# Kernel optimization log

Measured on AMD Instinct MI355X. Metric: run time of the kernel, lower is better.

## Reference

```python
import jax, jax.numpy as jnp
import numpy as np

N_NODES = 50000
N_EDGES = 800000
H = 128   # atom_hidden_feats
B = 64    # bond_in_feats
NEG_SLOPE = 0.01  # torch LeakyReLU default


def setup_inputs() -> dict:
    key = jax.random.key(0)
    k1, k2, k3, k4, k5 = jax.random.split(key, 5)
    feat = jax.random.normal(k1, (N_NODES, H), dtype=jnp.float32)
    gdf_feat = jax.random.normal(k2, (N_EDGES, B), dtype=jnp.float32)
    # Linear(2H+B -> H): weight [H, 2H+B], bias [H]
    W = jax.random.normal(k3, (H, 2 * H + B), dtype=jnp.float32) * 0.05
    b = jnp.zeros((H,), dtype=jnp.float32)
    src = jax.random.randint(k4, (N_EDGES,), 0, N_NODES, dtype=jnp.int64)
    dst = jax.random.randint(k5, (N_EDGES,), 0, N_NODES, dtype=jnp.int64)
    return {"feat": feat, "gdf_feat": gdf_feat, "W": W, "b": b, "src": src, "dst": dst}


def reference(feat, gdf_feat, W, b, src, dst):
    n_nodes = feat.shape[0]
    # Per-edge message: concat(src_feat, dst_feat, edge_feat) -> linear -> gate
    z = jnp.concatenate([feat[src], feat[dst], gdf_feat], axis=-1)  # [E, 2H+B]
    z = z @ W.T + b                                                 # [E, H]
    msg = jax.nn.sigmoid(z) * jnp.where(z > 0, z, NEG_SLOPE * z)    # sigmoid * leaky_relu
    # Scatter-sum messages to destination nodes
    return jax.ops.segment_sum(msg, dst, num_segments=n_nodes)      # [N, H]
```

## Files before the change

kernel.cpp:

```cpp
#include <hip/hip_runtime.h>
#include <hip/hip_bf16.h>

typedef __attribute__((ext_vector_type(8)))  short bf16x8;
typedef __attribute__((ext_vector_type(16))) float f32x16;
typedef __attribute__((ext_vector_type(4)))  float f32x4;
typedef __attribute__((ext_vector_type(2)))  __fp16 fp16x2;

#define NN 50000
#define EE 800000
#define HH 128
#define KK 320
#define NEG 0.01f
#define NTILES (EE / 64)
#define NBLK 1024
#define ACC_BYTES ((size_t)NN * HH * 2)

__device__ __forceinline__ unsigned pack2(float a, float b) {
    unsigned short lo = __builtin_bit_cast(unsigned short, __float2bfloat16(a));
    unsigned short hi = __builtin_bit_cast(unsigned short, __float2bfloat16(b));
    return (unsigned)lo | ((unsigned)hi << 16);
}

__global__ __launch_bounds__(256) void featcvt_kernel(const float* __restrict__ feat,
                                                      ushort* __restrict__ featb)
{
    const int t = blockIdx.x * 256 + threadIdx.x;
    const float* p = feat + (long long)t * 8;
    f32x4 v0 = *(const f32x4*)p;
    f32x4 v1 = *(const f32x4*)(p + 4);
    int4 h;
    h.x = (int)pack2(v0[0], v0[1]); h.y = (int)pack2(v0[2], v0[3]);
    h.z = (int)pack2(v1[0], v1[1]); h.w = (int)pack2(v1[2], v1[3]);
    *(int4*)(featb + (long long)t * 8) = h;
}

template<int USE_F16, int FEATB>
__global__ __launch_bounds__(256, 4) void fused_edge_kernel(
    const float*  __restrict__ feat, const ushort* __restrict__ featb,
    const float*  __restrict__ gdf,
    const float*  __restrict__ W,    const float* __restrict__ bias,
    const int*    __restrict__ src,  const int*   __restrict__ dst,
    float* __restrict__ out, __fp16* __restrict__ acc16)
{
    __shared__ int4 lds4[64 * 40];
    char* lds = (char*)lds4;

    const int tid  = threadIdx.x;
    const int lane = tid & 63;
    const int wid  = tid >> 6;
    const int col  = wid * 32 + (lane & 31);
    const int khalf = lane >> 5;
    const int r = tid >> 2, q = tid & 3;

    bf16x8 Wb[20];
    {
        const float* wrow = W + col * KK + khalf * 8;
        #pragma unroll
        for (int k = 0; k < 20; k++) {
            f32x4 x0 = *(const f32x4*)(wrow + k * 16);
            f32x4 x1 = *(const f32x4*)(wrow + k * 16 + 4);
            union { bf16x8 v; unsigned u[4]; } t;
            t.u[0] = pack2(x0[0], x0[1]); t.u[1] = pack2(x0[2], x0[3]);
            t.u[2] = pack2(x1[0], x1[1]); t.u[3] = pack2(x1[2], x1[3]);
            Wb[k] = t.v;
        }
    }
    const float bv = bias[col];

    int tile = blockIdx.x;
    int sCur = src[(long long)tile * 64 + r];
    int dCur = dst[(long long)tile * 64 + r];

    while (tile < NTILES) {
        const long long ebase = (long long)tile * 64;

        {
            const float* ge = gdf + (ebase + r) * 64;
            if (FEATB) {
                const ushort* fs = featb + (long long)sCur * HH;
                const ushort* fd = featb + (long long)dCur * HH;
                #pragma unroll
                for (int i = 0; i < 8; i++) {
                    const int c = q + i * 4;
                    const ushort* p = (c < 16) ? (fs + c * 8) : (fd + (c - 16) * 8);
                    int4 h = *(const int4*)p;
                    *(int4*)(lds + r * 640 + ((c * 16) ^ ((r & 7) << 4))) = h;
                }
                #pragma unroll
                for (int i = 8; i < 10; i++) {
                    const int c = q + i * 4;
                    const float* p = ge + (c - 32) * 8;
                    f32x4 v0 = *(const f32x4*)p;
                    f32x4 v1 = *(const f32x4*)(p + 4);
                    int4 h;
                    h.x = (int)pack2(v0[0], v0[1]); h.y = (int)pack2(v0[2], v0[3]);
                    h.z = (int)pack2(v1[0], v1[1]); h.w = (int)pack2(v1[2], v1[3]);
                    *(int4*)(lds + r * 640 + ((c * 16) ^ ((r & 7) << 4))) = h;
                }
            } else {
                const float* fs = feat + (long long)sCur * HH;
                const float* fd = feat + (long long)dCur * HH;
                #pragma unroll
                for (int i = 0; i < 10; i++) {
                    const int c = q + i * 4;
                    const float* p = (c < 16) ? (fs + c * 8)
                                   : (c < 32) ? (fd + (c - 16) * 8)
                                              : (ge + (c - 32) * 8);
                    f32x4 v0 = *(const f32x4*)p;
                    f32x4 v1 = *(const f32x4*)(p + 4);
                    int4 h;
                    h.x = (int)pack2(v0[0], v0[1]); h.y = (int)pack2(v0[2], v0[3]);
                    h.z = (int)pack2(v1[0], v1[1]); h.w = (int)pack2(v1[2], v1[3]);
                    *(int4*)(lds + r * 640 + ((c * 16) ^ ((r & 7) << 4))) = h;
                }
            }
        }
        __syncthreads();

        const int nt = tile + NBLK;
        if (nt < NTILES) {
            sCur = src[(long long)nt * 64 + r];
            dCur = dst[(long long)nt * 64 + r];
        }

        f32x16 acc0 = {}; f32x16 acc1 = {};
        const int arow = lane & 31;
        const int xr   = (arow & 7) << 4;
        #pragma unroll
        for (int k = 0; k < 20; k++) {
            const int kb = k * 32 + khalf * 16;
            bf16x8 a0 = *(const bf16x8*)(lds + arow * 640 + (kb ^ xr));
            bf16x8 a1 = *(const bf16x8*)(lds + (arow + 32) * 640 + (kb ^ xr));
            acc0 = __builtin_amdgcn_mfma_f32_32x32x16_bf16(a0, Wb[k], acc0, 0, 0, 0);
            acc1 = __builtin_amdgcn_mfma_f32_32x32x16_bf16(a1, Wb[k], acc1, 0, 0, 0);
        }

        const int* dtile = dst + ebase;
        #pragma unroll
        for (int rt = 0; rt < 2; rt++) {
            const f32x16 A = rt ? acc1 : acc0;
            #pragma unroll
            for (int g = 0; g < 4; g++) {
                #pragma unroll
                for (int j = 0; j < 4; j++) {
                    const int reg = g * 4 + j;
                    const int row = j + g * 8 + khalf * 4;
                    const float z  = A[reg] + bv;
                    const float lr = z > 0.f ? z : NEG * z;
                    const float sg = 1.f / (1.f + __expf(-z));
                    const float m  = lr * sg;
                    const int dn = dtile[rt * 32 + row];
                    if (USE_F16) {
                        const float o = __shfl_xor(m, 1);
                        if (!(lane & 1)) {
                            fp16x2 hv = __builtin_amdgcn_cvt_pkrtz(m, o);
                            __fp16* p = acc16 + (long long)dn * HH + col;
                            asm volatile("global_atomic_pk_add_f16 %0, %1, off"
                                         :: "v"(p), "v"(hv) : "memory");
                        }
                    } else {
                        unsafeAtomicAdd(out + (long long)dn * HH + col, m);
                    }
                }
            }
        }
        __syncthreads();
        tile = nt;
    }
}

__global__ __launch_bounds__(256) void conv_kernel(const int4* __restrict__ acc,
                                                   float4* __restrict__ out)
{
    const int i = blockIdx.x * 256 + threadIdx.x;
    union { int4 v; __fp16 h[8]; } u;
    u.v = acc[i];
    float4 a, b;
    a.x = (float)u.h[0]; a.y = (float)u.h[1]; a.z = (float)u.h[2]; a.w = (float)u.h[3];
    b.x = (float)u.h[4]; b.y = (float)u.h[5]; b.z = (float)u.h[6]; b.w = (float)u.h[7];
    out[2 * i]     = a;
    out[2 * i + 1] = b;
}

extern "C" void kernel_launch(void* const* d_in, const int* in_sizes, int n_in,
                              void* d_out, int out_size, void* d_ws, size_t ws_size,
                              hipStream_t stream) {
    const float* feat = (const float*)d_in[0];
    const float* gdf  = (const float*)d_in[1];
    const float* W    = (const float*)d_in[2];
    const float* bias = (const float*)d_in[3];
    const int*   src  = (const int*)d_in[4];
    const int*   dst  = (const int*)d_in[5];
    float* out = (float*)d_out;

    __fp16* acc16 = (__fp16*)d_ws;
    ushort* featb = (ushort*)((char*)d_ws + ACC_BYTES);

    if (ws_size >= 2 * ACC_BYTES) {
        (void)hipMemsetAsync(d_ws, 0, ACC_BYTES, stream);
        featcvt_kernel<<<(NN * HH / 8) / 256 + 1, 256, 0, stream>>>(feat, featb);
        fused_edge_kernel<1, 1><<<NBLK, 256, 0, stream>>>(feat, featb, gdf, W, bias,
                                                          src, dst, out, acc16);
        conv_kernel<<<(NN * HH / 8) / 256, 256, 0, stream>>>((const int4*)d_ws,
                                                             (float4*)out);
    } else if (ws_size >= ACC_BYTES) {
        (void)hipMemsetAsync(d_ws, 0, ACC_BYTES, stream);
        fused_edge_kernel<1, 0><<<NBLK, 256, 0, stream>>>(feat, featb, gdf, W, bias,
                                                          src, dst, out, acc16);
        conv_kernel<<<(NN * HH / 8) / 256, 256, 0, stream>>>((const int4*)d_ws,
                                                             (float4*)out);
    } else {
        (void)hipMemsetAsync(out, 0, (size_t)out_size * sizeof(float), stream);
        fused_edge_kernel<0, 0><<<NBLK, 256, 0, stream>>>(feat, featb, gdf, W, bias,
                                                          src, dst, out, acc16);
    }
}
```

Before: 395.2 us.

## Double-buffer edge tiles in LDS and prefetch next tile's gathers into registers

The persistent edge kernel becomes a software pipeline. The next tile's feature gathers and gdf loads go into registers while the current tile's MFMA and atomic scatter run, then get written into a second LDS buffer. Destination indices are staged in LDS instead of being reloaded from global memory in the epilogue. The block count is halved, the occupancy hint drops to 2 blocks per SM, and the fallback paths are simplified into a non-persistent kernel. Register and LDS pressure go up, and the smaller grid may hide latency less well.

After: 355.4 us. -10.1%, faster.

```diff
diff --git a/kernel.cpp b/kernel.cpp
--- a/kernel.cpp
+++ b/kernel.cpp
@@ -12,7 +12,7 @@
 #define KK 320
 #define NEG 0.01f
 #define NTILES (EE / 64)
-#define NBLK 1024
+#define NBLK 512
 #define ACC_BYTES ((size_t)NN * HH * 2)
 
 __device__ __forceinline__ unsigned pack2(float a, float b) {
@@ -34,16 +34,14 @@
     *(int4*)(featb + (long long)t * 8) = h;
 }
 
-template<int USE_F16, int FEATB>
-__global__ __launch_bounds__(256, 4) void fused_edge_kernel(
-    const float*  __restrict__ feat, const ushort* __restrict__ featb,
-    const float*  __restrict__ gdf,
-    const float*  __restrict__ W,    const float* __restrict__ bias,
-    const int*    __restrict__ src,  const int*   __restrict__ dst,
-    float* __restrict__ out, __fp16* __restrict__ acc16)
-{
-    __shared__ int4 lds4[64 * 40];
-    char* lds = (char*)lds4;
+__global__ __launch_bounds__(256, 2) void fused_pipe_kernel(
+    const ushort* __restrict__ featb, const float* __restrict__ gdf,
+    const float*  __restrict__ W,     const float* __restrict__ bias,
+    const int*    __restrict__ src,   const int*   __restrict__ dst,
+    __fp16* __restrict__ acc16)
+{
+    __shared__ int4 lds4[2][64 * 40];
+    __shared__ int  dsts[2][64];
 
     const int tid  = threadIdx.x;
     const int lane = tid & 63;
@@ -67,75 +65,87 @@
     }
     const float bv = bias[col];
 
+    int4  sf[8];
+    f32x4 sg[4];
+    int   dStage;
+
+    auto issueLoads = [&](int t, int s_i, int d_i) {
+        const ushort* fs = featb + (long long)s_i * HH;
+        const ushort* fd = featb + (long long)d_i * HH;
+        const float*  ge = gdf + ((long long)t * 64 + r) * 64;
+        #pragma unroll
+        for (int i = 0; i < 8; i++) {
+            const int c = q + i * 4;
+            sf[i] = *(const int4*)((c < 16) ? (fs + c * 8) : (fd + (c - 16) * 8));
+        }
+        #pragma unroll
+        for (int i = 0; i < 2; i++) {
+            const int cg = q + i * 4;
+            sg[2 * i]     = *(const f32x4*)(ge + cg * 8);
+            sg[2 * i + 1] = *(const f32x4*)(ge + cg * 8 + 4);
+        }
+    };
+    auto writeStage = [&](int buf) {
+        char* base = (char*)lds4[buf];
+        const int xr = (r & 7) << 4;
+        #pragma unroll
+        for (int i = 0; i < 8; i++) {
+            const int c = q + i * 4;
+            *(int4*)(base + r * 640 + ((c * 16) ^ xr)) = sf[i];
+        }
+        #pragma unroll
+        for (int i = 0; i < 2; i++) {
+            const int c = 32 + q + i * 4;
+            int4 h;
+            h.x = (int)pack2(sg[2*i][0], sg[2*i][1]);
+            h.y = (int)pack2(sg[2*i][2], sg[2*i][3]);
+            h.z = (int)pack2(sg[2*i+1][0], sg[2*i+1][1]);
+            h.w = (int)pack2(sg[2*i+1][2], sg[2*i+1][3]);
+            *(int4*)(base + r * 640 + ((c * 16) ^ xr)) = h;
+        }
+        if (q == 0) dsts[buf][r] = dStage;
+    };
+
     int tile = blockIdx.x;
-    int sCur = src[(long long)tile * 64 + r];
-    int dCur = dst[(long long)tile * 64 + r];
-
-    while (tile < NTILES) {
-        const long long ebase = (long long)tile * 64;
-
-        {
-            const float* ge = gdf + (ebase + r) * 64;
-            if (FEATB) {
-                const ushort* fs = featb + (long long)sCur * HH;
-                const ushort* fd = featb + (long long)dCur * HH;
-                #pragma unroll
-                for (int i = 0; i < 8; i++) {
-                    const int c = q + i * 4;
-                    const ushort* p = (c < 16) ? (fs + c * 8) : (fd + (c - 16) * 8);
-                    int4 h = *(const int4*)p;
-                    *(int4*)(lds + r * 640 + ((c * 16) ^ ((r & 7) << 4))) = h;
-                }
-                #pragma unroll
-                for (int i = 8; i < 10; i++) {
-                    const int c = q + i * 4;
-                    const float* p = ge + (c - 32) * 8;
-                    f32x4 v0 = *(const f32x4*)p;
-                    f32x4 v1 = *(const f32x4*)(p + 4);
-                    int4 h;
-                    h.x = (int)pack2(v0[0], v0[1]); h.y = (int)pack2(v0[2], v0[3]);
-                    h.z = (int)pack2(v1[0], v1[1]); h.w = (int)pack2(v1[2], v1[3]);
-                    *(int4*)(lds + r * 640 + ((c * 16) ^ ((r & 7) << 4))) = h;
-                }
-            } else {
-                const float* fs = feat + (long long)sCur * HH;
-                const float* fd = feat + (long long)dCur * HH;
-                #pragma unroll
-                for (int i = 0; i < 10; i++) {
-                    const int c = q + i * 4;
-                    const float* p = (c < 16) ? (fs + c * 8)
-                                   : (c < 32) ? (fd + (c - 16) * 8)
-                                              : (ge + (c - 32) * 8);
-                    f32x4 v0 = *(const f32x4*)p;
-                    f32x4 v1 = *(const f32x4*)(p + 4);
-                    int4 h;
-                    h.x = (int)pack2(v0[0], v0[1]); h.y = (int)pack2(v0[2], v0[3]);
-                    h.z = (int)pack2(v1[0], v1[1]); h.w = (int)pack2(v1[2], v1[3]);
-                    *(int4*)(lds + r * 640 + ((c * 16) ^ ((r & 7) << 4))) = h;
-                }
-            }
-        }
-        __syncthreads();
-
-        const int nt = tile + NBLK;
-        if (nt < NTILES) {
-            sCur = src[(long long)nt * 64 + r];
-            dCur = dst[(long long)nt * 64 + r];
-        }
-
+    int sN = src[(long long)tile * 64 + r];
+    int dN = dst[(long long)tile * 64 + r];
+    issueLoads(tile, sN, dN);
+    dStage = dN;
+    int nt = tile + NBLK;
+    {
+        const int tc = (nt < NTILES) ? nt : 0;
+        sN = src[(long long)tc * 64 + r];
+        dN = dst[(long long)tc * 64 + r];
+    }
+    writeStage(0);
+    __syncthreads();
+
+    int cur = 0;
+    const int arow = lane & 31;
+    const int xa   = (arow & 7) << 4;
+
+    while (true) {
+        const bool hasNext = (nt < NTILES);
+        if (hasNext) {
+            issueLoads(nt, sN, dN);
+            dStage = dN;
+            const int nnt = nt + NBLK;
+            const int tc = (nnt < NTILES) ? nnt : 0;
+            sN = src[(long long)tc * 64 + r];
+            dN = dst[(long long)tc * 64 + r];
+        }
+
+        char* abase = (char*)lds4[cur];
         f32x16 acc0 = {}; f32x16 acc1 = {};
-        const int arow = lane & 31;
-        const int xr   = (arow & 7) << 4;
         #pragma unroll
         for (int k = 0; k < 20; k++) {
             const int kb = k * 32 + khalf * 16;
-            bf16x8 a0 = *(const bf16x8*)(lds + arow * 640 + (kb ^ xr));
-            bf16x8 a1 = *(const bf16x8*)(lds + (arow + 32) * 640 + (kb ^ xr));
+            bf16x8 a0 = *(const bf16x8*)(abase + arow * 640 + (kb ^ xa));
+            bf16x8 a1 = *(const bf16x8*)(abase + (arow + 32) * 640 + (kb ^ xa));
             acc0 = __builtin_amdgcn_mfma_f32_32x32x16_bf16(a0, Wb[k], acc0, 0, 0, 0);
             acc1 = __builtin_amdgcn_mfma_f32_32x32x16_bf16(a1, Wb[k], acc1, 0, 0, 0);
         }
 
-        const int* dtile = dst + ebase;
         #pragma unroll
         for (int rt = 0; rt < 2; rt++) {
             const f32x16 A = rt ? acc1 : acc0;
@@ -147,25 +157,101 @@
                     const int row = j + g * 8 + khalf * 4;
                     const float z  = A[reg] + bv;
                     const float lr = z > 0.f ? z : NEG * z;
-                    const float sg = 1.f / (1.f + __expf(-z));
-                    const float m  = lr * sg;
-                    const int dn = dtile[rt * 32 + row];
-                    if (USE_F16) {
-                        const float o = __shfl_xor(m, 1);
-                        if (!(lane & 1)) {
-                            fp16x2 hv = __builtin_amdgcn_cvt_pkrtz(m, o);
-                            __fp16* p = acc16 + (long long)dn * HH + col;
-                            asm volatile("global_atomic_pk_add_f16 %0, %1, off"
-                                         :: "v"(p), "v"(hv) : "memory");
-                        }
-                    } else {
-                        unsafeAtomicAdd(out + (long long)dn * HH + col, m);
+                    const float sg2 = 1.f / (1.f + __expf(-z));
+                    const float m  = lr * sg2;
+                    const float o  = __shfl_xor(m, 1);
+                    const int dn = dsts[cur][rt * 32 + row];
+                    if (!(lane & 1)) {
+                        fp16x2 hv = __builtin_amdgcn_cvt_pkrtz(m, o);
+                        __fp16* p = acc16 + (long long)dn * HH + col;
+                        asm volatile("global_atomic_pk_add_f16 %0, %1, off"
+                                     :: "v"(p), "v"(hv) : "memory");
                     }
                 }
             }
         }
+
+        if (!hasNext) break;
+        writeStage(cur ^ 1);
+        tile = nt; nt += NBLK; cur ^= 1;
         __syncthreads();
-        tile = nt;
+    }
+}
+
+__global__ __launch_bounds__(256) void fused_fallback_kernel(
+    const float* __restrict__ feat, const float* __restrict__ gdf,
+    const float* __restrict__ W,    const float* __restrict__ bias,
+    const int*   __restrict__ src,  const int*   __restrict__ dst,
+    float* __restrict__ out)
+{
+    __shared__ int4 lds4[64 * 40];
+    __shared__ int  dsts[64];
+    char* lds = (char*)lds4;
+    const int tid = threadIdx.x, lane = tid & 63, wid = tid >> 6;
+    const int col = wid * 32 + (lane & 31), khalf = lane >> 5;
+    const int r = tid >> 2, q = tid & 3;
+    const long long ebase = (long long)blockIdx.x * 64;
+
+    bf16x8 Wb[20];
+    {
+        const float* wrow = W + col * KK + khalf * 8;
+        #pragma unroll
+        for (int k = 0; k < 20; k++) {
+            f32x4 x0 = *(const f32x4*)(wrow + k * 16);
+            f32x4 x1 = *(const f32x4*)(wrow + k * 16 + 4);
+            union { bf16x8 v; unsigned u[4]; } t;
+            t.u[0] = pack2(x0[0], x0[1]); t.u[1] = pack2(x0[2], x0[3]);
+            t.u[2] = pack2(x1[0], x1[1]); t.u[3] = pack2(x1[2], x1[3]);
+            Wb[k] = t.v;
+        }
+    }
+    const int s = src[ebase + r], d = dst[ebase + r];
+    if (q == 0) dsts[r] = d;
+    {
+        const float* fs = feat + (long long)s * HH;
+        const float* fd = feat + (long long)d * HH;
+        const float* ge = gdf + (ebase + r) * 64;
+        #pragma unroll
+        for (int i = 0; i < 10; i++) {
+            const int c = q + i * 4;
+            const float* p = (c < 16) ? (fs + c * 8)
+                           : (c < 32) ? (fd + (c - 16) * 8)
+                                      : (ge + (c - 32) * 8);
+            f32x4 v0 = *(const f32x4*)p;
+            f32x4 v1 = *(const f32x4*)(p + 4);
+            int4 h;
+            h.x = (int)pack2(v0[0], v0[1]); h.y = (int)pack2(v0[2], v0[3]);
+            h.z = (int)pack2(v1[0], v1[1]); h.w = (int)pack2(v1[2], v1[3]);
+            *(int4*)(lds + r * 640 + ((c * 16) ^ ((r & 7) << 4))) = h;
+        }
+    }
+    __syncthreads();
+    f32x16 acc0 = {}; f32x16 acc1 = {};
+    const int arow = lane & 31, xa = (arow & 7) << 4;
+    #pragma unroll
+    for (int k = 0; k < 20; k++) {
+        const int kb = k * 32 + khalf * 16;
+        bf16x8 a0 = *(const bf16x8*)(lds + arow * 640 + (kb ^ xa));
+        bf16x8 a1 = *(const bf16x8*)(lds + (arow + 32) * 640 + (kb ^ xa));
+        acc0 = __builtin_amdgcn_mfma_f32_32x32x16_bf16(a0, Wb[k], acc0, 0, 0, 0);
+        acc1 = __builtin_amdgcn_mfma_f32_32x32x16_bf16(a1, Wb[k], acc1, 0, 0, 0);
+    }
+    const float bv = bias[col];
+    #pragma unroll
+    for (int rt = 0; rt < 2; rt++) {
+        const f32x16 A = rt ? acc1 : acc0;
+        #pragma unroll
+        for (int g = 0; g < 4; g++) {
+            #pragma unroll
+            for (int j = 0; j < 4; j++) {
+                const int reg = g * 4 + j;
+                const int row = j + g * 8 + khalf * 4;
+                const float z  = A[reg] + bv;
+                const float lr = z > 0.f ? z : NEG * z;
+                const float sgm = 1.f / (1.f + __expf(-z));
+                unsafeAtomicAdd(out + (long long)dsts[rt * 32 + row] * HH + col, lr * sgm);
+            }
+        }
     }
 }
 
@@ -198,20 +284,14 @@
 
     if (ws_size >= 2 * ACC_BYTES) {
         (void)hipMemsetAsync(d_ws, 0, ACC_BYTES, stream);
-        featcvt_kernel<<<(NN * HH / 8) / 256 + 1, 256, 0, stream>>>(feat, featb);
-        fused_edge_kernel<1, 1><<<NBLK, 256, 0, stream>>>(feat, featb, gdf, W, bias,
-                                                          src, dst, out, acc16);
-        conv_kernel<<<(NN * HH / 8) / 256, 256, 0, stream>>>((const int4*)d_ws,
-                                                             (float4*)out);
-    } else if (ws_size >= ACC_BYTES) {
-        (void)hipMemsetAsync(d_ws, 0, ACC_BYTES, stream);
-        fused_edge_kernel<1, 0><<<NBLK, 256, 0, stream>>>(feat, featb, gdf, W, bias,
-                                                          src, dst, out, acc16);
-        conv_kernel<<<(NN * HH / 8) / 256, 256, 0, stream>>>((const int4*)d_ws,
-                                                             (float4*)out);
+        featcvt_kernel<<<NN * HH / 8 / 256, 256, 0, stream>>>(feat, featb);
+        fused_pipe_kernel<<<NBLK, 256, 0, stream>>>(featb, gdf, W, bias,
+                                                    src, dst, acc16);
+        conv_kernel<<<NN * HH / 8 / 256, 256, 0, stream>>>((const int4*)d_ws,
+                                                           (float4*)out);
     } else {
         (void)hipMemsetAsync(out, 0, (size_t)out_size * sizeof(float), stream);
-        fused_edge_kernel<0, 0><<<NBLK, 256, 0, stream>>>(feat, featb, gdf, W, bias,
-                                                          src, dst, out, acc16);
-    }
-}
+        fused_fallback_kernel<<<EE / 64, 256, 0, stream>>>(feat, gdf, W, bias,
+                                                           src, dst, out);
+    }
+}
```
